# Optimization experiments

Hardware: AMD Instinct MI355X
Metric: run time of the kernel (lower is better)

The kernel has to match this reference:

```python
import jax, jax.numpy as jnp
import numpy as np
from math import sqrt

D_MODEL = 1024
N_HEADS = 16
FFN = 4096
B, N = 2, 2048
EPS = 1e-5


def _layernorm(x, g, b):
    mu = jnp.mean(x, -1, keepdims=True)
    var = jnp.mean((x - mu) ** 2, -1, keepdims=True)
    return (x - mu) * jax.lax.rsqrt(var + EPS) * g + b


def setup_inputs() -> dict:
    key = jax.random.key(0)
    ks = jax.random.split(key, 12)
    s = 1.0 / sqrt(D_MODEL)
    sf = 1.0 / sqrt(FFN)
    inp = {
        "tgt": jax.random.normal(ks[0], (B, N, D_MODEL), jnp.float32),
        # True = masked. Causal: query i may attend to keys j <= i.
        "tgt_mask": jnp.triu(jnp.ones((N, N), jnp.bool_), k=1),
        "tgt_key_pad_mask": jnp.zeros((B, N), jnp.bool_),
        "Wq": jax.random.uniform(ks[1], (D_MODEL, D_MODEL), jnp.float32, -s, s),
        "Wk": jax.random.uniform(ks[2], (D_MODEL, D_MODEL), jnp.float32, -s, s),
        "Wv": jax.random.uniform(ks[3], (D_MODEL, D_MODEL), jnp.float32, -s, s),
        "Wo": jax.random.uniform(ks[4], (D_MODEL, D_MODEL), jnp.float32, -s, s),
        "bo": jax.random.uniform(ks[5], (D_MODEL,), jnp.float32, -s, s),
        "W1": jax.random.uniform(ks[6], (FFN, D_MODEL), jnp.float32, -s, s),
        "b1": jax.random.uniform(ks[7], (FFN,), jnp.float32, -s, s),
        "W2": jax.random.uniform(ks[8], (D_MODEL, FFN), jnp.float32, -sf, sf),
        "b2": jax.random.uniform(ks[9], (D_MODEL,), jnp.float32, -sf, sf),
        "g1": jnp.ones((D_MODEL,), jnp.float32),
        "beta1": jnp.zeros((D_MODEL,), jnp.float32),
        "g2": jnp.ones((D_MODEL,), jnp.float32),
        "beta2": jnp.zeros((D_MODEL,), jnp.float32),
    }
    return inp


def _mha(x, tgt_mask, pad_mask, Wq, Wk, Wv, Wo, bo):
    b, n, d = x.shape
    dk = d // N_HEADS
    q = (x @ Wq.T).reshape(b, n, N_HEADS, dk).transpose(0, 2, 1, 3)  # bhnd
    k = (x @ Wk.T).reshape(b, n, N_HEADS, dk).transpose(0, 2, 1, 3)
    v = (x @ Wv.T).reshape(b, n, N_HEADS, dk).transpose(0, 2, 1, 3)
    scores = jnp.einsum("bhqd,bhkd->bhqk", q, k) / sqrt(dk)
    mask = tgt_mask[None, None, :, :] | pad_mask[:, None, None, :]
    scores = jnp.where(mask, -jnp.inf, scores)
    att = jax.nn.softmax(scores, axis=-1)
    out = jnp.einsum("bhqk,bhkd->bhqd", att, v).transpose(0, 2, 1, 3).reshape(b, n, d)
    return out @ Wo.T + bo


def reference(tgt, tgt_mask, tgt_key_pad_mask, Wq, Wk, Wv, Wo, bo,
              W1, b1, W2, b2, g1, beta1, g2, beta2):
    # PostNorm logic (pre_norm=False), dropout=0 (eval)
    h = _mha(tgt, tgt_mask, tgt_key_pad_mask, Wq, Wk, Wv, Wo, bo)
    x = _layernorm(tgt + h, g1, beta1)
    m = jax.nn.gelu(x @ W1.T + b1, approximate=True) @ W2.T + b2
    return _layernorm(x + m, g2, beta2)
```

## Files before the change

### kernel.cpp

```cpp
#include <hip/hip_runtime.h>


#define DEV __device__ __forceinline__

typedef __attribute__((ext_vector_type(4)))  float f32x4;
typedef __attribute__((ext_vector_type(16))) float f32x16;
typedef __attribute__((ext_vector_type(8)))  short s16x8;

static constexpr int Bb   = 2;
static constexpr int NN   = 2048;
static constexpr int DM   = 1024;
static constexpr int HH   = 16;
static constexpr int DK   = 64;
static constexpr int FF   = 4096;
static constexpr int ROWS = Bb * NN;

#define AS1(p) ((const __attribute__((address_space(1))) void*)(p))
#define AS3(p) ((__attribute__((address_space(3))) void*)(p))

DEV unsigned short f2bf(float f) {
  unsigned u = __float_as_uint(f);
  u += 0x7fff + ((u >> 16) & 1);
  return (unsigned short)(u >> 16);
}
DEV unsigned pack2bf(float lo, float hi) {
  return (unsigned)f2bf(lo) | ((unsigned)f2bf(hi) << 16);
}

__global__ __launch_bounds__(256) void k_cast(const float* __restrict__ in,
                                              ushort* __restrict__ out, int n4) {
  int i = blockIdx.x * 256 + threadIdx.x;
  if (i >= n4) return;
  float4 v = reinterpret_cast<const float4*>(in)[i];
  ushort4 o;
  o.x = f2bf(v.x); o.y = f2bf(v.y); o.z = f2bf(v.z); o.w = f2bf(v.w);
  reinterpret_cast<ushort4*>(out)[i] = o;
}

template <int EPI, int BN, bool QKV>
__global__ __launch_bounds__(256) void k_gemm(
    const ushort* __restrict__ A, const ushort* __restrict__ Bt,
    const float* __restrict__ bias, const float* __restrict__ resid,
    ushort* __restrict__ Cb, float* __restrict__ Cf,
    int K, int nbx) {
  __shared__ ushort As[2][128][32];
  __shared__ ushort Bs[2][BN][32];

  const int t = threadIdx.x;
  const int lane = t & 63, w = t >> 6;
  const int lr = lane & 15, lg = lane >> 4;
  const int lrow = lane >> 2, lc8 = (lane & 3) * 8;

  const int nwg = gridDim.x;
  const int bid = blockIdx.x;
  const int q8 = nwg >> 3, r8 = nwg & 7;
  const int xcd = bid & 7, lin = bid >> 3;
  const int wg = (xcd < r8 ? xcd * (q8 + 1) : r8 * (q8 + 1) + (xcd - r8) * q8) + lin;
  const int band = wg / (4 * nbx);
  const int inn  = wg % (4 * nbx);
  const int by = band * 4 + (inn & 3);
  const int bx = inn >> 2;

  const int bRow = by * 128;
  const int bCol = bx * BN;

  constexpr int NW = BN / 32;
  const int wRow = (w >> 1) * 64, wCol = (w & 1) * (BN / 2);

  const f32x4 zero = {0.f, 0.f, 0.f, 0.f};
  f32x4 acc[4][NW];
#pragma unroll
  for (int m = 0; m < 4; ++m)
#pragma unroll
    for (int n = 0; n < NW; ++n) acc[m][n] = zero;

  auto stage = [&](int buf, int kt) {
#pragma unroll
    for (int i = 0; i < 2; ++i) {
      int rr = w * 32 + i * 16;
      __builtin_amdgcn_global_load_lds(
          AS1(A + (size_t)(bRow + rr + lrow) * K + kt + lc8),
          AS3(&As[buf][rr][0]), 16, 0, 0);
    }
#pragma unroll
    for (int i = 0; i < BN / 64; ++i) {
      int rr = w * (BN / 4) + i * 16;
      __builtin_amdgcn_global_load_lds(
          AS1(Bt + (size_t)(bCol + rr + lrow) * K + kt + lc8),
          AS3(&Bs[buf][rr][0]), 16, 0, 0);
    }
  };

  stage(0, 0);
  const int nk = K / 32;
  for (int tt = 0; tt < nk; ++tt) {
    const int cur = tt & 1;
    __syncthreads();
    if (tt + 1 < nk) stage(cur ^ 1, (tt + 1) * 32);

    s16x8 af[4], bfr[NW];
#pragma unroll
    for (int m = 0; m < 4; ++m)
      af[m] = *reinterpret_cast<const s16x8*>(&As[cur][wRow + m * 16 + lr][lg * 8]);
#pragma unroll
    for (int n = 0; n < NW; ++n)
      bfr[n] = *reinterpret_cast<const s16x8*>(&Bs[cur][wCol + n * 16 + lr][lg * 8]);
#pragma unroll
    for (int m = 0; m < 4; ++m)
#pragma unroll
      for (int n = 0; n < NW; ++n)
        acc[m][n] = __builtin_amdgcn_mfma_f32_16x16x32_bf16(af[m], bfr[n], acc[m][n], 0, 0, 0);
  }

  ushort* CbOut = Cb;
  int colBase = bCol, Ncols = nbx * BN;
  if (QKV) {
    CbOut = Cb + (size_t)(bCol >> 10) * ROWS * DM;
    colBase = bCol & 1023;
    Ncols = DM;
  }
#pragma unroll
  for (int m = 0; m < 4; ++m) {
    int gr = bRow + wRow + m * 16 + lg * 4;
#pragma unroll
    for (int n = 0; n < NW; ++n) {
      int gc = colBase + wCol + n * 16 + lr;
      float bv = (EPI == 1 || EPI == 2) ? bias[gc] : 0.0f;
#pragma unroll
      for (int r = 0; r < 4; ++r) {
        size_t idx = (size_t)(gr + r) * Ncols + gc;
        float v = acc[m][n][r] + bv;
        if (EPI == 2) {
          Cf[idx] = v + resid[idx];
        } else if (EPI == 1) {
          float u = v + 0.044715f * v * v * v;
          float g = v / (1.0f + __expf(-1.5957691216057308f * u));
          CbOut[idx] = f2bf(g);
        } else {
          CbOut[idx] = f2bf(v);
        }
      }
    }
  }
}

template <int WB>
__global__ __launch_bounds__(256) void k_ln(const float* __restrict__ in,
                                            const float* __restrict__ g,
                                            const float* __restrict__ bta,
                                            float* __restrict__ outf,
                                            ushort* __restrict__ outb) {
  const int row = blockIdx.x;
  const int t = threadIdx.x;
  float4 v = reinterpret_cast<const float4*>(in + (size_t)row * DM)[t];
  float s1 = v.x + v.y + v.z + v.w;
  float s2 = v.x * v.x + v.y * v.y + v.z * v.z + v.w * v.w;
#pragma unroll
  for (int m = 32; m; m >>= 1) {
    s1 += __shfl_xor(s1, m, 64);
    s2 += __shfl_xor(s2, m, 64);
  }
  __shared__ float red[2][4];
  if ((t & 63) == 0) { red[0][t >> 6] = s1; red[1][t >> 6] = s2; }
  __syncthreads();
  s1 = red[0][0] + red[0][1] + red[0][2] + red[0][3];
  s2 = red[1][0] + red[1][1] + red[1][2] + red[1][3];
  const float mu = s1 * (1.0f / DM);
  const float var = s2 * (1.0f / DM) - mu * mu;
  const float rstd = rsqrtf(var + 1e-5f);
  float4 gv = reinterpret_cast<const float4*>(g)[t];
  float4 bv = reinterpret_cast<const float4*>(bta)[t];
  float4 o;
  o.x = (v.x - mu) * rstd * gv.x + bv.x;
  o.y = (v.y - mu) * rstd * gv.y + bv.y;
  o.z = (v.z - mu) * rstd * gv.z + bv.z;
  o.w = (v.w - mu) * rstd * gv.w + bv.w;
  reinterpret_cast<float4*>(outf + (size_t)row * DM)[t] = o;
  if (WB) {
    ushort4 ob;
    ob.x = f2bf(o.x); ob.y = f2bf(o.y); ob.z = f2bf(o.z); ob.w = f2bf(o.w);
    reinterpret_cast<ushort4*>(outb + (size_t)row * DM)[t] = ob;
  }
}

__global__ __launch_bounds__(256) void k_attn(const ushort* __restrict__ Q,
                                              const ushort* __restrict__ Kb,
                                              const ushort* __restrict__ Vb,
                                              ushort* __restrict__ O) {
  __shared__ ushort Ks[64 * 64];
  __shared__ ushort Vt[64][72];

  const int t = threadIdx.x;
  const int qi = (NN / 128 - 1) - (int)blockIdx.x;
  const int bh = blockIdx.y;
  const int b = bh >> 4, h = bh & 15;
  const int lane = t & 63, wid = t >> 6;
  const int l31 = lane & 31, hi = lane >> 5;
  const int q0w = qi * 128 + wid * 32;
  const size_t base = ((size_t)b * NN) * DM + h * DK;

  char* KsB = (char*)Ks;

  s16x8 qf[4];
#pragma unroll
  for (int c = 0; c < 4; ++c)
    qf[c] = *reinterpret_cast<const s16x8*>(Q + base + (size_t)(q0w + l31) * DM + c * 16 + hi * 8);

  float mrun = -1e30f, lrun = 0.f;
  f32x16 accO[2];
#pragma unroll
  for (int dt = 0; dt < 2; ++dt)
#pragma unroll
    for (int r = 0; r < 16; ++r) accO[dt][r] = 0.f;

  const int srow = t >> 2;
  const int sc4  = t & 3;

  const int nkt = 2 * qi + 2;
  for (int kt = 0; kt < nkt; ++kt) {
    const int kk = kt * 64;
#pragma unroll
    for (int hh = 0; hh < 2; ++hh) {
      int co = sc4 * 16 + hh * 64;
      int4 kv = *reinterpret_cast<const int4*>(Kb + base + (size_t)(kk + srow) * DM + (co >> 1));
      *reinterpret_cast<int4*>(KsB + srow * 128 + (co ^ ((srow & 7) << 4))) = kv;
      int d0 = sc4 * 8 + hh * 32;
      int4 vv = *reinterpret_cast<const int4*>(Vb + base + (size_t)(kk + srow) * DM + d0);
      ushort vs[8];
      *reinterpret_cast<int4*>(vs) = vv;
#pragma unroll
      for (int j = 0; j < 8; ++j) Vt[d0 + j][srow] = vs[j];
    }
    __syncthreads();

    if (kk <= q0w + 31) {
      f32x16 st[2];
#pragma unroll
      for (int sub = 0; sub < 2; ++sub) {
#pragma unroll
        for (int r = 0; r < 16; ++r) st[sub][r] = 0.f;
        const int row = sub * 32 + l31;
        const int swz = (row & 7) << 4;
#pragma unroll
        for (int c = 0; c < 4; ++c) {
          s16x8 kf = *reinterpret_cast<const s16x8*>(KsB + row * 128 + ((c * 32 + hi * 16) ^ swz));
          st[sub] = __builtin_amdgcn_mfma_f32_32x32x16_bf16(kf, qf[c], st[sub], 0, 0, 0);
        }
      }

      const int q = q0w + l31;
      const bool needmask = (kk + 63 > q0w);
      float p[32];
      float rm = -1e30f;
#pragma unroll
      for (int sub = 0; sub < 2; ++sub)
#pragma unroll
        for (int r = 0; r < 16; ++r) {
          int kl = sub * 32 + (r & 3) + 8 * (r >> 2) + 4 * hi;
          float v = st[sub][r] * 0.125f;
          if (needmask && (kk + kl > q)) v = -1e30f;
          p[sub * 16 + r] = v;
          rm = fmaxf(rm, v);
        }
      rm = fmaxf(rm, __shfl_xor(rm, 32, 64));
      const float mn = fmaxf(mrun, rm);
      const float alpha = __expf(mrun - mn);
      mrun = mn;
      float rs = 0.f;
#pragma unroll
      for (int i = 0; i < 32; ++i) { p[i] = __expf(p[i] - mn); rs += p[i]; }
      rs += __shfl_xor(rs, 32, 64);
      lrun = lrun * alpha + rs;
#pragma unroll
      for (int dt = 0; dt < 2; ++dt) accO[dt] *= alpha;

      s16x8 pf[4];
#pragma unroll
      for (int sub = 0; sub < 2; ++sub)
#pragma unroll
        for (int half = 0; half < 2; ++half) {
          const float* pp = &p[sub * 16 + half * 8];
          unsigned X0 = pack2bf(pp[0], pp[1]);
          unsigned X1 = pack2bf(pp[2], pp[3]);
          unsigned Y0 = pack2bf(pp[4], pp[5]);
          unsigned Y1 = pack2bf(pp[6], pp[7]);
          asm volatile("v_permlane32_swap_b32 %0, %1" : "+v"(X0), "+v"(Y0));
          asm volatile("v_permlane32_swap_b32 %0, %1" : "+v"(X1), "+v"(Y1));
          union { unsigned u[4]; s16x8 v; } uu;
          uu.u[0] = X0; uu.u[1] = X1; uu.u[2] = Y0; uu.u[3] = Y1;
          pf[sub * 2 + half] = uu.v;
        }

#pragma unroll
      for (int dt = 0; dt < 2; ++dt) {
        const int d = dt * 32 + l31;
#pragma unroll
        for (int kc = 0; kc < 4; ++kc) {
          s16x8 vf = *reinterpret_cast<const s16x8*>(&Vt[d][kc * 16 + hi * 8]);
          accO[dt] = __builtin_amdgcn_mfma_f32_32x32x16_bf16(vf, pf[kc], accO[dt], 0, 0, 0);
        }
      }
    }
    __syncthreads();
  }

  const int q = q0w + l31;
  const float inv = 1.0f / lrun;
#pragma unroll
  for (int dt = 0; dt < 2; ++dt)
#pragma unroll
    for (int rg = 0; rg < 4; ++rg) {
      int d0 = 8 * rg + 4 * hi + 32 * dt;
      ushort4 ov;
      ov.x = f2bf(accO[dt][rg * 4 + 0] * inv);
      ov.y = f2bf(accO[dt][rg * 4 + 1] * inv);
      ov.z = f2bf(accO[dt][rg * 4 + 2] * inv);
      ov.w = f2bf(accO[dt][rg * 4 + 3] * inv);
      *reinterpret_cast<ushort4*>(O + base + (size_t)q * DM + d0) = ov;
    }
}

extern "C" void kernel_launch(void* const* d_in, const int* in_sizes, int n_in,
                              void* d_out, int out_size, void* d_ws, size_t ws_size,
                              hipStream_t stream) {
  const float* tgt = (const float*)d_in[0];
  const float* Wq  = (const float*)d_in[3];
  const float* Wk  = (const float*)d_in[4];
  const float* Wv  = (const float*)d_in[5];
  const float* Wo  = (const float*)d_in[6];
  const float* bo  = (const float*)d_in[7];
  const float* W1  = (const float*)d_in[8];
  const float* b1  = (const float*)d_in[9];
  const float* W2  = (const float*)d_in[10];
  const float* b2  = (const float*)d_in[11];
  const float* g1  = (const float*)d_in[12];
  const float* be1 = (const float*)d_in[13];
  const float* g2  = (const float*)d_in[14];
  const float* be2 = (const float*)d_in[15];

  char* ws = (char*)d_ws;
  size_t off = 0;
  auto alloc = [&](size_t bytes) {
    void* p = ws + off;
    off += (bytes + 255) & ~(size_t)255;
    return p;
  };
  ushort* xb   = (ushort*)alloc((size_t)ROWS * DM * 2);
  ushort* wqb  = (ushort*)alloc((size_t)DM * DM * 2);
  ushort* wkb  = (ushort*)alloc((size_t)DM * DM * 2);
  ushort* wvb  = (ushort*)alloc((size_t)DM * DM * 2);
  ushort* wob  = (ushort*)alloc((size_t)DM * DM * 2);
  ushort* w1b  = (ushort*)alloc((size_t)FF * DM * 2);
  ushort* w2b  = (ushort*)alloc((size_t)DM * FF * 2);
  ushort* qbuf = (ushort*)alloc((size_t)ROWS * DM * 2);
  ushort* kbuf = (ushort*)alloc((size_t)ROWS * DM * 2);
  ushort* vbuf = (ushort*)alloc((size_t)ROWS * DM * 2);
  ushort* atnb = (ushort*)alloc((size_t)ROWS * DM * 2);
  float*  h1   = (float*)alloc((size_t)ROWS * DM * 4);
  float*  x1f  = (float*)alloc((size_t)ROWS * DM * 4);
  ushort* x1b  = (ushort*)alloc((size_t)ROWS * DM * 2);
  ushort* t1b  = (ushort*)alloc((size_t)ROWS * FF * 2);
  (void)ws_size; (void)in_sizes; (void)n_in; (void)out_size;
  (void)wkb; (void)wvb; (void)kbuf; (void)vbuf;

  auto cast = [&](const float* src, ushort* dst, size_t n) {
    int n4 = (int)(n / 4);
    k_cast<<<dim3((n4 + 255) / 256), 256, 0, stream>>>(src, dst, n4);
  };
  cast(tgt, xb, (size_t)ROWS * DM);
  cast(Wq, wqb, (size_t)DM * DM);
  cast(Wk, wkb, (size_t)DM * DM);
  cast(Wv, wvb, (size_t)DM * DM);
  cast(Wo, wob, (size_t)DM * DM);
  cast(W1, w1b, (size_t)FF * DM);
  cast(W2, w2b, (size_t)DM * FF);

  dim3 blk(256);
  k_gemm<0, 128, true><<<dim3(24 * 32), blk, 0, stream>>>(
      xb, wqb, nullptr, nullptr, qbuf, nullptr, DM, 24);

  k_attn<<<dim3(NN / 128, Bb * HH), blk, 0, stream>>>(qbuf, kbuf, vbuf, atnb);

  k_gemm<2, 64, false><<<dim3(16 * 32), blk, 0, stream>>>(
      atnb, wob, bo, tgt, nullptr, h1, DM, 16);
  k_ln<1><<<dim3(ROWS), blk, 0, stream>>>(h1, g1, be1, x1f, x1b);

  k_gemm<1, 128, false><<<dim3(32 * 32), blk, 0, stream>>>(
      x1b, w1b, b1, nullptr, t1b, nullptr, DM, 32);
  float* z = h1;
  k_gemm<2, 64, false><<<dim3(16 * 32), blk, 0, stream>>>(
      t1b, w2b, b2, x1f, nullptr, z, FF, 16);
  k_ln<0><<<dim3(ROWS), blk, 0, stream>>>(z, g2, be2, (float*)d_out, nullptr);
}
```

Baseline: 304.8 us.

## Double-buffer attention K/V via async LDS loads with pre-transposed swizzled V

The QKV GEMM epilogue now writes K with an XOR swizzle. A new kernel pre-transposes V into a per-head swizzled layout, so attention can stream K and V tiles straight into double-buffered LDS with global_load_lds and skip the per-thread scalar transpose. This removes one barrier per tile. The softmax now uses exp2 with the scale folded in, and rescales only when the running max changes. Diagonal tiles skip the half-masked subtile, and bf16 packing uses the hardware cvt_pk instruction. The cost is an extra transpose kernel and workspace buffer, and the code depends on the swizzle layouts matching across kernels.

```diff
diff --git a/kernel.cpp b/kernel.cpp
--- a/kernel.cpp
+++ b/kernel.cpp
@@ -23,8 +23,15 @@
   u += 0x7fff + ((u >> 16) & 1);
   return (unsigned short)(u >> 16);
 }
-DEV unsigned pack2bf(float lo, float hi) {
-  return (unsigned)f2bf(lo) | ((unsigned)f2bf(hi) << 16);
+DEV float fexp2(float x) {
+  float r;
+  asm("v_exp_f32 %0, %1" : "=v"(r) : "v"(x));
+  return r;
+}
+DEV unsigned cvtpk(float lo, float hi) {
+  unsigned r;
+  asm("v_cvt_pk_bf16_f32 %0, %1, %2" : "=v"(r) : "v"(lo), "v"(hi));
+  return r;
 }
 
 __global__ __launch_bounds__(256) void k_cast(const float* __restrict__ in,
@@ -113,9 +120,10 @@
   }
 
   ushort* CbOut = Cb;
-  int colBase = bCol, Ncols = nbx * BN;
+  int colBase = bCol, Ncols = nbx * BN, third = 0;
   if (QKV) {
-    CbOut = Cb + (size_t)(bCol >> 10) * ROWS * DM;
+    third = bCol >> 10;
+    CbOut = Cb + (size_t)third * ROWS * DM;
     colBase = bCol & 1023;
     Ncols = DM;
   }
@@ -128,19 +136,52 @@
       float bv = (EPI == 1 || EPI == 2) ? bias[gc] : 0.0f;
 #pragma unroll
       for (int r = 0; r < 4; ++r) {
-        size_t idx = (size_t)(gr + r) * Ncols + gc;
+        int nr = gr + r;
         float v = acc[m][n][r] + bv;
         if (EPI == 2) {
+          size_t idx = (size_t)nr * Ncols + gc;
           Cf[idx] = v + resid[idx];
         } else if (EPI == 1) {
+          size_t idx = (size_t)nr * Ncols + gc;
           float u = v + 0.044715f * v * v * v;
           float g = v / (1.0f + __expf(-1.5957691216057308f * u));
           CbOut[idx] = f2bf(g);
         } else {
-          CbOut[idx] = f2bf(v);
+          int gcs = gc;
+          if (QKV && third == 1)
+            gcs = (gc & ~63) | ((gc ^ ((nr & 7) << 3)) & 63);
+          CbOut[(size_t)nr * Ncols + gcs] = f2bf(v);
         }
       }
     }
+  }
+}
+
+__global__ __launch_bounds__(256) void k_vt(const ushort* __restrict__ V,
+                                            ushort* __restrict__ vT) {
+  __shared__ ushort Ls[64][72];
+  const int t = threadIdx.x;
+  const int n0 = blockIdx.x * 64;
+  const int bh = blockIdx.y;
+  const int b = bh >> 4, h = bh & 15;
+  const int n = t >> 2;
+#pragma unroll
+  for (int half = 0; half < 2; ++half) {
+    int c8 = ((t & 3) + half * 4) * 8;
+    int4 v = *reinterpret_cast<const int4*>(
+        V + ((size_t)(b * NN + n0 + n)) * DM + h * DK + c8);
+    *reinterpret_cast<int4*>(&Ls[n][c8]) = v;
+  }
+  __syncthreads();
+  const int d = t >> 2;
+#pragma unroll
+  for (int half = 0; half < 2; ++half) {
+    int c = (t & 3) + half * 4;
+    ushort tmp[8];
+#pragma unroll
+    for (int j = 0; j < 8; ++j) tmp[j] = Ls[c * 8 + j][d];
+    size_t out = ((size_t)bh * DK + d) * NN + n0 + ((c ^ (d & 7)) * 8);
+    *reinterpret_cast<int4*>(vT + out) = *reinterpret_cast<const int4*>(tmp);
   }
 }
 
@@ -185,58 +226,68 @@
 
 __global__ __launch_bounds__(256) void k_attn(const ushort* __restrict__ Q,
                                               const ushort* __restrict__ Kb,
-                                              const ushort* __restrict__ Vb,
+                                              const ushort* __restrict__ vT,
                                               ushort* __restrict__ O) {
-  __shared__ ushort Ks[64 * 64];
-  __shared__ ushort Vt[64][72];
+  __shared__ ushort Ks[2][64 * 64];
+  __shared__ ushort Vs[2][64 * 64];
 
   const int t = threadIdx.x;
   const int qi = (NN / 128 - 1) - (int)blockIdx.x;
   const int bh = blockIdx.y;
-  const int b = bh >> 4, h = bh & 15;
   const int lane = t & 63, wid = t >> 6;
   const int l31 = lane & 31, hi = lane >> 5;
   const int q0w = qi * 128 + wid * 32;
-  const size_t base = ((size_t)b * NN) * DM + h * DK;
-
-  char* KsB = (char*)Ks;
+  const size_t base = (size_t)bh * NN * DM / HH * HH;
+  const size_t qbase = ((size_t)(bh >> 4) * NN) * DM + (bh & 15) * DK;
+  const size_t vbase = (size_t)bh * DK * NN;
+  (void)base;
+
+  const float C = 0.18033688011112043f;
 
   s16x8 qf[4];
 #pragma unroll
   for (int c = 0; c < 4; ++c)
-    qf[c] = *reinterpret_cast<const s16x8*>(Q + base + (size_t)(q0w + l31) * DM + c * 16 + hi * 8);
-
-  float mrun = -1e30f, lrun = 0.f;
+    qf[c] = *reinterpret_cast<const s16x8*>(Q + qbase + (size_t)(q0w + l31) * DM + c * 16 + hi * 8);
+
+  float mrun = -1e30f, lrun = 0.f, negcm = 1e30f;
   f32x16 accO[2];
 #pragma unroll
   for (int dt = 0; dt < 2; ++dt)
 #pragma unroll
     for (int r = 0; r < 16; ++r) accO[dt][r] = 0.f;
 
-  const int srow = t >> 2;
-  const int sc4  = t & 3;
+  auto stage = [&](int buf, int kt) {
+    const int kk = kt * 64;
+#pragma unroll
+    for (int i = 0; i < 2; ++i) {
+      int row0 = wid * 16 + i * 8;
+      __builtin_amdgcn_global_load_lds(
+          AS1(Kb + qbase + (size_t)(kk + row0 + (lane >> 3)) * DM + (lane & 7) * 8),
+          AS3(&Ks[buf][row0 * 64]), 16, 0, 0);
+      __builtin_amdgcn_global_load_lds(
+          AS1(vT + vbase + (size_t)(row0 + (lane >> 3)) * NN + kk + (lane & 7) * 8),
+          AS3(&Vs[buf][row0 * 64]), 16, 0, 0);
+    }
+  };
 
   const int nkt = 2 * qi + 2;
+  stage(0, 0);
   for (int kt = 0; kt < nkt; ++kt) {
+    const int cur = kt & 1;
     const int kk = kt * 64;
-#pragma unroll
-    for (int hh = 0; hh < 2; ++hh) {
-      int co = sc4 * 16 + hh * 64;
-      int4 kv = *reinterpret_cast<const int4*>(Kb + base + (size_t)(kk + srow) * DM + (co >> 1));
-      *reinterpret_cast<int4*>(KsB + srow * 128 + (co ^ ((srow & 7) << 4))) = kv;
-      int d0 = sc4 * 8 + hh * 32;
-      int4 vv = *reinterpret_cast<const int4*>(Vb + base + (size_t)(kk + srow) * DM + d0);
-      ushort vs[8];
-      *reinterpret_cast<int4*>(vs) = vv;
-#pragma unroll
-      for (int j = 0; j < 8; ++j) Vt[d0 + j][srow] = vs[j];
-    }
     __syncthreads();
+    if (kt + 1 < nkt) stage(cur ^ 1, kt + 1);
 
     if (kk <= q0w + 31) {
+      const char* KsB = (const char*)Ks[cur];
+      const char* VsB = (const char*)Vs[cur];
+      const bool diag = (kk + 64 > q0w);
+      const int nsub = (kk + 32 <= q0w + 31) ? 2 : 1;
+
       f32x16 st[2];
 #pragma unroll
       for (int sub = 0; sub < 2; ++sub) {
+        if (sub >= nsub) break;
 #pragma unroll
         for (int r = 0; r < 16; ++r) st[sub][r] = 0.f;
         const int row = sub * 32 + l31;
@@ -249,59 +300,85 @@
       }
 
       const int q = q0w + l31;
-      const bool needmask = (kk + 63 > q0w);
       float p[32];
-      float rm = -1e30f;
-#pragma unroll
-      for (int sub = 0; sub < 2; ++sub)
+#pragma unroll
+      for (int sub = 0; sub < 2; ++sub) {
+        if (sub >= nsub) break;
 #pragma unroll
         for (int r = 0; r < 16; ++r) {
-          int kl = sub * 32 + (r & 3) + 8 * (r >> 2) + 4 * hi;
-          float v = st[sub][r] * 0.125f;
-          if (needmask && (kk + kl > q)) v = -1e30f;
+          float v = st[sub][r];
+          if (diag) {
+            int kl = sub * 32 + (r & 3) + 8 * (r >> 2) + 4 * hi;
+            if (kk + kl > q) v = -1e30f;
+          }
           p[sub * 16 + r] = v;
-          rm = fmaxf(rm, v);
         }
-      rm = fmaxf(rm, __shfl_xor(rm, 32, 64));
-      const float mn = fmaxf(mrun, rm);
-      const float alpha = __expf(mrun - mn);
-      mrun = mn;
-      float rs = 0.f;
-#pragma unroll
-      for (int i = 0; i < 32; ++i) { p[i] = __expf(p[i] - mn); rs += p[i]; }
-      rs += __shfl_xor(rs, 32, 64);
-      lrun = lrun * alpha + rs;
-#pragma unroll
-      for (int dt = 0; dt < 2; ++dt) accO[dt] *= alpha;
+      }
+      float a[16];
+#pragma unroll
+      for (int i = 0; i < 16; ++i) a[i] = (nsub == 2) ? fmaxf(p[i], p[i + 16]) : p[i];
+#pragma unroll
+      for (int s = 8; s; s >>= 1)
+#pragma unroll
+        for (int i = 0; i < 8; ++i) if (i < s) a[i] = fmaxf(a[i], a[i + s]);
+      float rm = fmaxf(a[0], __shfl_xor(a[0], 32, 64));
+
+      if (__any(rm > mrun)) {
+        const float mn = fmaxf(mrun, rm);
+        const float alpha = fexp2(C * (mrun - mn));
+        mrun = mn;
+        negcm = -C * mn;
+        lrun *= alpha;
+#pragma unroll
+        for (int dt = 0; dt < 2; ++dt) accO[dt] *= alpha;
+      }
+
+#pragma unroll
+      for (int sub = 0; sub < 2; ++sub) {
+        if (sub >= nsub) break;
+#pragma unroll
+        for (int i = 0; i < 16; ++i)
+          p[sub * 16 + i] = fexp2(fmaf(p[sub * 16 + i], C, negcm));
+      }
+#pragma unroll
+      for (int i = 0; i < 16; ++i) a[i] = (nsub == 2) ? (p[i] + p[i + 16]) : p[i];
+#pragma unroll
+      for (int s = 8; s; s >>= 1)
+#pragma unroll
+        for (int i = 0; i < 8; ++i) if (i < s) a[i] += a[i + s];
+      lrun += a[0] + __shfl_xor(a[0], 32, 64);
 
       s16x8 pf[4];
 #pragma unroll
-      for (int sub = 0; sub < 2; ++sub)
+      for (int sub = 0; sub < 2; ++sub) {
+        if (sub >= nsub) break;
 #pragma unroll
         for (int half = 0; half < 2; ++half) {
           const float* pp = &p[sub * 16 + half * 8];
-          unsigned X0 = pack2bf(pp[0], pp[1]);
-          unsigned X1 = pack2bf(pp[2], pp[3]);
-          unsigned Y0 = pack2bf(pp[4], pp[5]);
-          unsigned Y1 = pack2bf(pp[6], pp[7]);
+          unsigned X0 = cvtpk(pp[0], pp[1]);
+          unsigned X1 = cvtpk(pp[2], pp[3]);
+          unsigned Y0 = cvtpk(pp[4], pp[5]);
+          unsigned Y1 = cvtpk(pp[6], pp[7]);
           asm volatile("v_permlane32_swap_b32 %0, %1" : "+v"(X0), "+v"(Y0));
           asm volatile("v_permlane32_swap_b32 %0, %1" : "+v"(X1), "+v"(Y1));
           union { unsigned u[4]; s16x8 v; } uu;
           uu.u[0] = X0; uu.u[1] = X1; uu.u[2] = Y0; uu.u[3] = Y1;
           pf[sub * 2 + half] = uu.v;
         }
+      }
 
 #pragma unroll
       for (int dt = 0; dt < 2; ++dt) {
         const int d = dt * 32 + l31;
+        const int vswz = (d & 7) << 4;
 #pragma unroll
         for (int kc = 0; kc < 4; ++kc) {
-          s16x8 vf = *reinterpret_cast<const s16x8*>(&Vt[d][kc * 16 + hi * 8]);
+          if (kc >= nsub * 2) break;
+          s16x8 vf = *reinterpret_cast<const s16x8*>(VsB + d * 128 + ((kc * 32 + hi * 16) ^ vswz));
           accO[dt] = __builtin_amdgcn_mfma_f32_32x32x16_bf16(vf, pf[kc], accO[dt], 0, 0, 0);
         }
       }
     }
-    __syncthreads();
   }
 
   const int q = q0w + l31;
@@ -316,7 +393,7 @@
       ov.y = f2bf(accO[dt][rg * 4 + 1] * inv);
       ov.z = f2bf(accO[dt][rg * 4 + 2] * inv);
       ov.w = f2bf(accO[dt][rg * 4 + 3] * inv);
-      *reinterpret_cast<ushort4*>(O + base + (size_t)q * DM + d0) = ov;
+      *reinterpret_cast<ushort4*>(O + qbase + (size_t)q * DM + d0) = ov;
     }
 }
 
@@ -355,13 +432,14 @@
   ushort* qbuf = (ushort*)alloc((size_t)ROWS * DM * 2);
   ushort* kbuf = (ushort*)alloc((size_t)ROWS * DM * 2);
   ushort* vbuf = (ushort*)alloc((size_t)ROWS * DM * 2);
+  ushort* vtb  = (ushort*)alloc((size_t)ROWS * DM * 2);
   ushort* atnb = (ushort*)alloc((size_t)ROWS * DM * 2);
   float*  h1   = (float*)alloc((size_t)ROWS * DM * 4);
   float*  x1f  = (float*)alloc((size_t)ROWS * DM * 4);
   ushort* x1b  = (ushort*)alloc((size_t)ROWS * DM * 2);
   ushort* t1b  = (ushort*)alloc((size_t)ROWS * FF * 2);
   (void)ws_size; (void)in_sizes; (void)n_in; (void)out_size;
-  (void)wkb; (void)wvb; (void)kbuf; (void)vbuf;
+  (void)wkb; (void)wvb; (void)kbuf;
 
   auto cast = [&](const float* src, ushort* dst, size_t n) {
     int n4 = (int)(n / 4);
@@ -379,7 +457,9 @@
   k_gemm<0, 128, true><<<dim3(24 * 32), blk, 0, stream>>>(
       xb, wqb, nullptr, nullptr, qbuf, nullptr, DM, 24);
 
-  k_attn<<<dim3(NN / 128, Bb * HH), blk, 0, stream>>>(qbuf, kbuf, vbuf, atnb);
+  k_vt<<<dim3(NN / 64, Bb * HH), blk, 0, stream>>>(vbuf, vtb);
+
+  k_attn<<<dim3(NN / 128, Bb * HH), blk, 0, stream>>>(qbuf, kbuf, vtb, atnb);
 
   k_gemm<2, 64, false><<<dim3(16 * 32), blk, 0, stream>>>(
       atnb, wob, bo, tgt, nullptr, h1, DM, 16);
```

Measured after the change: 305.3 us. About the same (+0.2%).
